# Kernel tuning notes

Measured on AMD Instinct MI355X. Metric: run time of the kernel, lower is better.

## Reference

```python
import jax, jax.numpy as jnp
import numpy as np

DIM = 1024
B, S = 4, 4096

def setup_inputs() -> dict:
    key = jax.random.key(0)
    ks = jax.random.split(key, 8)
    scale = 1.0 / np.sqrt(DIM)
    x = jax.random.normal(ks[0], (B, S, DIM), dtype=jnp.float32)
    Wk = jax.random.normal(ks[1], (DIM, DIM), dtype=jnp.float32) * scale
    Wv = jax.random.normal(ks[2], (DIM, DIM), dtype=jnp.float32) * scale
    Wr = jax.random.normal(ks[3], (DIM, DIM), dtype=jnp.float32) * scale
    Wo = jax.random.normal(ks[4], (DIM, DIM), dtype=jnp.float32) * scale
    time_decay = jax.random.normal(ks[5], (DIM,), dtype=jnp.float32) * 0.01 - 5.0
    time_first = jax.random.normal(ks[6], (DIM,), dtype=jnp.float32) * 0.01
    return {"x": x, "Wk": Wk, "Wv": Wv, "Wr": Wr, "Wo": Wo,
            "time_decay": time_decay, "time_first": time_first}

def reference(x, Wk, Wv, Wr, Wo, time_decay, time_first):
    # Projections (Linear with weight [out, in]: y = x @ W^T)
    k = jnp.einsum('bsd,ed->bse', x, Wk)
    v = jnp.einsum('bsd,ed->bse', x, Wv)
    r = jax.nn.sigmoid(jnp.einsum('bsd,ed->bse', x, Wr))
    w = -jnp.exp(time_decay)          # (D,)
    decay = jnp.exp(w)                # exp(w), per-channel decay in (0,1)
    eu = jnp.exp(time_first)          # exp(u)
    kv = k * v                        # (B, S, D)

    def step(state, kv_t):
        wkv = state + eu * kv_t       # output numerator this step
        new_state = decay * state + kv_t
        return new_state, wkv

    state0 = jnp.zeros((x.shape[0], x.shape[2]), dtype=x.dtype)
    # scan over time axis: move S to leading dim
    _, wkv_seq = jax.lax.scan(step, state0, jnp.swapaxes(kv, 0, 1))  # (S, B, D)
    out = r * jnp.swapaxes(wkv_seq, 0, 1)  # (B, S, D)
    return jnp.einsum('bsd,ed->bse', out, Wo)
```

## Files before the change

### kernel.cpp

```cpp
#include <hip/hip_runtime.h>
#include <hip/hip_bf16.h>

#define DIMD   1024
#define BATCH  4
#define SEQ    4096
#define NTOK   (BATCH * SEQ)
#define CHUNK  64
#define NCHUNK (SEQ / CHUNK)

#define BM 128
#define BN 128
#define BK 32

typedef unsigned short ushort_t;
typedef __attribute__((ext_vector_type(8))) __bf16   bf16x8;
typedef __attribute__((ext_vector_type(4))) float    f32x4;
typedef __attribute__((ext_vector_type(8))) ushort_t u16x8;

__device__ __forceinline__ float b2f(ushort_t u) {
    union { unsigned int i; float f; } x;
    x.i = ((unsigned int)u) << 16;
    return x.f;
}

__device__ __forceinline__ ushort_t f2b(float f) {
    union { float f; unsigned int i; } x;
    x.f = f;
    unsigned int r = x.i + 0x7fffu + ((x.i >> 16) & 1u);
    return (ushort_t)(r >> 16);
}

__global__ __launch_bounds__(256)
void conv_f2b(const float* __restrict__ src, ushort_t* __restrict__ dst, int n8)
{
    const int i = blockIdx.x * 256 + threadIdx.x;
    if (i >= n8) return;
    const float4* s4 = (const float4*)src;
    const float4 a = s4[i * 2];
    const float4 b = s4[i * 2 + 1];
    u16x8 o;
    o[0] = f2b(a.x); o[1] = f2b(a.y); o[2] = f2b(a.z); o[3] = f2b(a.w);
    o[4] = f2b(b.x); o[5] = f2b(b.y); o[6] = f2b(b.z); o[7] = f2b(b.w);
    *(u16x8*)(dst + (size_t)i * 8) = o;
}

__global__ __launch_bounds__(256, 2)
void gemm_kv(const ushort_t* __restrict__ A,
             const ushort_t* __restrict__ Wk,
             const ushort_t* __restrict__ Wv,
             ushort_t* __restrict__ Okv)
{
    __shared__ __align__(16) ushort_t As[BM * BK];
    __shared__ __align__(16) ushort_t Bk[BN * BK];
    __shared__ __align__(16) ushort_t Bv[BN * BK];

    const int tid  = threadIdx.x;
    const int lane = tid & 63;
    const int wv   = tid >> 6;
    const int wr   = wv >> 1;
    const int wc   = wv & 1;
    const int lrow = lane & 15;
    const int kq   = lane >> 4;

    const int row0 = blockIdx.x * BM;
    const int e0   = blockIdx.y * BN;

    f32x4 ak[4][4], av[4][4];
#pragma unroll
    for (int i = 0; i < 4; i++)
#pragma unroll
        for (int j = 0; j < 4; j++) {
            ak[i][j] = f32x4{0.f, 0.f, 0.f, 0.f};
            av[i][j] = f32x4{0.f, 0.f, 0.f, 0.f};
        }

    for (int kt = 0; kt < DIMD / BK; ++kt) {
        const int k0 = kt * BK;

        __syncthreads();

#pragma unroll
        for (int it = 0; it < 2; ++it) {
            const int chunk = tid + it * 256;
            const int r = chunk >> 2;
            const int c = (chunk & 3) << 3;
            const ushort_t* ga = A  + (size_t)(row0 + r) * DIMD + k0 + c;
            const ushort_t* gk = Wk + (size_t)(e0 + r) * DIMD + k0 + c;
            const ushort_t* gv = Wv + (size_t)(e0 + r) * DIMD + k0 + c;
            __builtin_amdgcn_global_load_lds(
                (__attribute__((address_space(1))) void*)ga,
                (__attribute__((address_space(3))) void*)((char*)As + chunk * 16),
                16, 0, 0);
            __builtin_amdgcn_global_load_lds(
                (__attribute__((address_space(1))) void*)gk,
                (__attribute__((address_space(3))) void*)((char*)Bk + chunk * 16),
                16, 0, 0);
            __builtin_amdgcn_global_load_lds(
                (__attribute__((address_space(1))) void*)gv,
                (__attribute__((address_space(3))) void*)((char*)Bv + chunk * 16),
                16, 0, 0);
        }

        __syncthreads();

        bf16x8 af[4], bk4[4], bv4[4];
#pragma unroll
        for (int i = 0; i < 4; i++)
            af[i] = *(const bf16x8*)(As + (wr * 64 + i * 16 + lrow) * BK + kq * 8);
#pragma unroll
        for (int j = 0; j < 4; j++) {
            bk4[j] = *(const bf16x8*)(Bk + (wc * 64 + j * 16 + lrow) * BK + kq * 8);
            bv4[j] = *(const bf16x8*)(Bv + (wc * 64 + j * 16 + lrow) * BK + kq * 8);
        }

#pragma unroll
        for (int i = 0; i < 4; i++)
#pragma unroll
            for (int j = 0; j < 4; j++) {
                ak[i][j] = __builtin_amdgcn_mfma_f32_16x16x32_bf16(
                    af[i], bk4[j], ak[i][j], 0, 0, 0);
                av[i][j] = __builtin_amdgcn_mfma_f32_16x16x32_bf16(
                    af[i], bv4[j], av[i][j], 0, 0, 0);
            }
    }

#pragma unroll
    for (int i = 0; i < 4; i++)
#pragma unroll
        for (int j = 0; j < 4; j++)
#pragma unroll
            for (int r = 0; r < 4; r++) {
                const int row = row0 + wr * 64 + i * 16 + kq * 4 + r;
                const int col = e0 + wc * 64 + j * 16 + lrow;
                Okv[(size_t)row * DIMD + col] = f2b(ak[i][j][r] * av[i][j][r]);
            }
}

template <int SIG, int F32OUT>
__global__ __launch_bounds__(256, 2)
void gemm_bt(const ushort_t* __restrict__ A,
             const ushort_t* __restrict__ W,
             ushort_t* __restrict__ Ob,
             float* __restrict__ Of)
{
    __shared__ __align__(16) ushort_t As[BM * BK];
    __shared__ __align__(16) ushort_t Bs[BN * BK];

    const int tid  = threadIdx.x;
    const int lane = tid & 63;
    const int wv   = tid >> 6;
    const int wr   = wv >> 1;
    const int wc   = wv & 1;
    const int lrow = lane & 15;
    const int kq   = lane >> 4;

    const int row0 = blockIdx.x * BM;
    const int e0   = blockIdx.y * BN;

    f32x4 acc[4][4];
#pragma unroll
    for (int i = 0; i < 4; i++)
#pragma unroll
        for (int j = 0; j < 4; j++)
            acc[i][j] = f32x4{0.f, 0.f, 0.f, 0.f};

    for (int kt = 0; kt < DIMD / BK; ++kt) {
        const int k0 = kt * BK;

        __syncthreads();

#pragma unroll
        for (int it = 0; it < 2; ++it) {
            const int chunk = tid + it * 256;
            const int r = chunk >> 2;
            const int c = (chunk & 3) << 3;
            const ushort_t* ga = A + (size_t)(row0 + r) * DIMD + k0 + c;
            const ushort_t* gb = W + (size_t)(e0 + r) * DIMD + k0 + c;
            __builtin_amdgcn_global_load_lds(
                (__attribute__((address_space(1))) void*)ga,
                (__attribute__((address_space(3))) void*)((char*)As + chunk * 16),
                16, 0, 0);
            __builtin_amdgcn_global_load_lds(
                (__attribute__((address_space(1))) void*)gb,
                (__attribute__((address_space(3))) void*)((char*)Bs + chunk * 16),
                16, 0, 0);
        }

        __syncthreads();

        bf16x8 af[4], bfr[4];
#pragma unroll
        for (int i = 0; i < 4; i++)
            af[i] = *(const bf16x8*)(As + (wr * 64 + i * 16 + lrow) * BK + kq * 8);
#pragma unroll
        for (int j = 0; j < 4; j++)
            bfr[j] = *(const bf16x8*)(Bs + (wc * 64 + j * 16 + lrow) * BK + kq * 8);

#pragma unroll
        for (int i = 0; i < 4; i++)
#pragma unroll
            for (int j = 0; j < 4; j++)
                acc[i][j] = __builtin_amdgcn_mfma_f32_16x16x32_bf16(
                    af[i], bfr[j], acc[i][j], 0, 0, 0);
    }

#pragma unroll
    for (int i = 0; i < 4; i++)
#pragma unroll
        for (int j = 0; j < 4; j++)
#pragma unroll
            for (int r = 0; r < 4; r++) {
                const int row = row0 + wr * 64 + i * 16 + kq * 4 + r;
                const int col = e0 + wc * 64 + j * 16 + lrow;
                float val = acc[i][j][r];
                if (F32OUT) {
                    Of[(size_t)row * DIMD + col] = val;
                } else {
                    if (SIG) val = 1.f / (1.f + __expf(-val));
                    Ob[(size_t)row * DIMD + col] = f2b(val);
                }
            }
}

__global__ __launch_bounds__(256)
void chunk_agg(const ushort_t* __restrict__ kvb,
               const float* __restrict__ td, float* __restrict__ cs)
{
    const int idx = blockIdx.x * 256 + threadIdx.x;
    const int d  = idx & (DIMD - 1);
    const int bc = idx >> 10;
    const int c  = bc & (NCHUNK - 1);
    const int b  = bc >> 6;

    const float decay = __expf(-__expf(td[d]));

    size_t off = ((size_t)b * SEQ + (size_t)c * CHUNK) * DIMD + d;
    float s = 0.f;
#pragma unroll 8
    for (int i = 0; i < CHUNK; i++) {
        s = decay * s + b2f(kvb[off]);
        off += DIMD;
    }
    cs[idx] = s;
}

__global__ __launch_bounds__(256)
void chunk_scan(float* __restrict__ cs, const float* __restrict__ td)
{
    const int idx = blockIdx.x * 256 + threadIdx.x;
    const int d = idx & (DIMD - 1);
    const int b = idx >> 10;

    const float w      = -__expf(td[d]);
    const float decayL = __expf(w * (float)CHUNK);

    float st = 0.f;
    for (int c = 0; c < NCHUNK; c++) {
        const size_t o = ((size_t)b * NCHUNK + c) * DIMD + d;
        const float sc = cs[o];
        cs[o] = st;
        st = decayL * st + sc;
    }
}

__global__ __launch_bounds__(256)
void emit(const ushort_t* __restrict__ kvb, const ushort_t* __restrict__ rb,
          const float* __restrict__ td, const float* __restrict__ tf,
          const float* __restrict__ cs, ushort_t* __restrict__ op)
{
    const int idx = blockIdx.x * 256 + threadIdx.x;
    const int d  = idx & (DIMD - 1);
    const int bc = idx >> 10;
    const int c  = bc & (NCHUNK - 1);
    const int b  = bc >> 6;

    const float decay = __expf(-__expf(td[d]));
    const float eu    = __expf(tf[d]);

    float st = cs[idx];
    size_t off = ((size_t)b * SEQ + (size_t)c * CHUNK) * DIMD + d;
#pragma unroll 8
    for (int i = 0; i < CHUNK; i++) {
        const float kv = b2f(kvb[off]);
        const float rr = b2f(rb[off]);
        op[off] = f2b(rr * (st + eu * kv));
        st = decay * st + kv;
        off += DIMD;
    }
}

extern "C" void kernel_launch(void* const* d_in, const int* in_sizes, int n_in,
                              void* d_out, int out_size, void* d_ws, size_t ws_size,
                              hipStream_t stream)
{
    const float* x  = (const float*)d_in[0];
    const float* Wk = (const float*)d_in[1];
    const float* Wv = (const float*)d_in[2];
    const float* Wr = (const float*)d_in[3];
    const float* Wo = (const float*)d_in[4];
    const float* td = (const float*)d_in[5];
    const float* tf = (const float*)d_in[6];

    ushort_t* xb   = (ushort_t*)d_ws;
    ushort_t* Wkb  = xb  + (size_t)NTOK * DIMD;
    ushort_t* Wvb  = Wkb + (size_t)DIMD * DIMD;
    ushort_t* Wrb  = Wvb + (size_t)DIMD * DIMD;
    ushort_t* Wob  = Wrb + (size_t)DIMD * DIMD;
    float*    cs   = (float*)(Wob + (size_t)DIMD * DIMD);
    ushort_t* pbuf = xb;

    ushort_t* kvb = (ushort_t*)d_out;
    ushort_t* rb  = kvb + (size_t)NTOK * DIMD;
    float*    out = (float*)d_out;

    conv_f2b<<<(NTOK * DIMD / 8 + 255) / 256, 256, 0, stream>>>(x, xb, NTOK * DIMD / 8);
    conv_f2b<<<(DIMD * DIMD / 8 + 255) / 256, 256, 0, stream>>>(Wk, Wkb, DIMD * DIMD / 8);
    conv_f2b<<<(DIMD * DIMD / 8 + 255) / 256, 256, 0, stream>>>(Wv, Wvb, DIMD * DIMD / 8);
    conv_f2b<<<(DIMD * DIMD / 8 + 255) / 256, 256, 0, stream>>>(Wr, Wrb, DIMD * DIMD / 8);
    conv_f2b<<<(DIMD * DIMD / 8 + 255) / 256, 256, 0, stream>>>(Wo, Wob, DIMD * DIMD / 8);

    gemm_kv<<<dim3(NTOK / BM, DIMD / BN), 256, 0, stream>>>(xb, Wkb, Wvb, kvb);

    gemm_bt<1, 0><<<dim3(NTOK / BM, DIMD / BN), 256, 0, stream>>>(xb, Wrb, rb, nullptr);

    chunk_agg<<<(BATCH * NCHUNK * DIMD) / 256, 256, 0, stream>>>(kvb, td, cs);

    chunk_scan<<<(BATCH * DIMD) / 256, 256, 0, stream>>>(cs, td);

    emit<<<(BATCH * NCHUNK * DIMD) / 256, 256, 0, stream>>>(kvb, rb, td, tf, cs, pbuf);

    gemm_bt<0, 1><<<dim3(NTOK / BM, DIMD / BN), 256, 0, stream>>>(pbuf, Wob, nullptr, out);
}
```

Measured before the change: 331.5 us.

## Fuse r projection into kv GEMM, batch weight conversion, vectorize scan kernels

```diff
diff --git a/kernel.cpp b/kernel.cpp
--- a/kernel.cpp
+++ b/kernel.cpp
@@ -44,15 +44,35 @@
     *(u16x8*)(dst + (size_t)i * 8) = o;
 }
 
+__global__ __launch_bounds__(256)
+void conv_w(const float* __restrict__ W0, const float* __restrict__ W1,
+            const float* __restrict__ W2, const float* __restrict__ W3,
+            ushort_t* __restrict__ dst)
+{
+    const int m = blockIdx.y;
+    const float* src = (m == 0) ? W0 : (m == 1) ? W1 : (m == 2) ? W2 : W3;
+    const int i = blockIdx.x * 256 + threadIdx.x;
+    const float4* s4 = (const float4*)src;
+    const float4 a = s4[i * 2];
+    const float4 b = s4[i * 2 + 1];
+    u16x8 o;
+    o[0] = f2b(a.x); o[1] = f2b(a.y); o[2] = f2b(a.z); o[3] = f2b(a.w);
+    o[4] = f2b(b.x); o[5] = f2b(b.y); o[6] = f2b(b.z); o[7] = f2b(b.w);
+    *(u16x8*)(dst + (size_t)m * DIMD * DIMD + (size_t)i * 8) = o;
+}
+
 __global__ __launch_bounds__(256, 2)
-void gemm_kv(const ushort_t* __restrict__ A,
-             const ushort_t* __restrict__ Wk,
-             const ushort_t* __restrict__ Wv,
-             ushort_t* __restrict__ Okv)
+void gemm_kvr(const ushort_t* __restrict__ A,
+              const ushort_t* __restrict__ Wk,
+              const ushort_t* __restrict__ Wv,
+              const ushort_t* __restrict__ Wr,
+              ushort_t* __restrict__ Okv,
+              ushort_t* __restrict__ Or)
 {
     __shared__ __align__(16) ushort_t As[BM * BK];
     __shared__ __align__(16) ushort_t Bk[BN * BK];
     __shared__ __align__(16) ushort_t Bv[BN * BK];
+    __shared__ __align__(16) ushort_t Br[BN * BK];
 
     const int tid  = threadIdx.x;
     const int lane = tid & 63;
@@ -65,13 +85,14 @@
     const int row0 = blockIdx.x * BM;
     const int e0   = blockIdx.y * BN;
 
-    f32x4 ak[4][4], av[4][4];
+    f32x4 ak[4][4], av[4][4], ar[4][4];
 #pragma unroll
     for (int i = 0; i < 4; i++)
 #pragma unroll
         for (int j = 0; j < 4; j++) {
             ak[i][j] = f32x4{0.f, 0.f, 0.f, 0.f};
             av[i][j] = f32x4{0.f, 0.f, 0.f, 0.f};
+            ar[i][j] = f32x4{0.f, 0.f, 0.f, 0.f};
         }
 
     for (int kt = 0; kt < DIMD / BK; ++kt) {
@@ -87,6 +108,7 @@
             const ushort_t* ga = A  + (size_t)(row0 + r) * DIMD + k0 + c;
             const ushort_t* gk = Wk + (size_t)(e0 + r) * DIMD + k0 + c;
             const ushort_t* gv = Wv + (size_t)(e0 + r) * DIMD + k0 + c;
+            const ushort_t* gr = Wr + (size_t)(e0 + r) * DIMD + k0 + c;
             __builtin_amdgcn_global_load_lds(
                 (__attribute__((address_space(1))) void*)ga,
                 (__attribute__((address_space(3))) void*)((char*)As + chunk * 16),
@@ -99,11 +121,15 @@
                 (__attribute__((address_space(1))) void*)gv,
                 (__attribute__((address_space(3))) void*)((char*)Bv + chunk * 16),
                 16, 0, 0);
+            __builtin_amdgcn_global_load_lds(
+                (__attribute__((address_space(1))) void*)gr,
+                (__attribute__((address_space(3))) void*)((char*)Br + chunk * 16),
+                16, 0, 0);
         }
 
         __syncthreads();
 
-        bf16x8 af[4], bk4[4], bv4[4];
+        bf16x8 af[4], bk4[4], bv4[4], br4[4];
 #pragma unroll
         for (int i = 0; i < 4; i++)
             af[i] = *(const bf16x8*)(As + (wr * 64 + i * 16 + lrow) * BK + kq * 8);
@@ -111,6 +137,7 @@
         for (int j = 0; j < 4; j++) {
             bk4[j] = *(const bf16x8*)(Bk + (wc * 64 + j * 16 + lrow) * BK + kq * 8);
             bv4[j] = *(const bf16x8*)(Bv + (wc * 64 + j * 16 + lrow) * BK + kq * 8);
+            br4[j] = *(const bf16x8*)(Br + (wc * 64 + j * 16 + lrow) * BK + kq * 8);
         }
 
 #pragma unroll
@@ -121,6 +148,8 @@
                     af[i], bk4[j], ak[i][j], 0, 0, 0);
                 av[i][j] = __builtin_amdgcn_mfma_f32_16x16x32_bf16(
                     af[i], bv4[j], av[i][j], 0, 0, 0);
+                ar[i][j] = __builtin_amdgcn_mfma_f32_16x16x32_bf16(
+                    af[i], br4[j], ar[i][j], 0, 0, 0);
             }
     }
 
@@ -132,15 +161,15 @@
             for (int r = 0; r < 4; r++) {
                 const int row = row0 + wr * 64 + i * 16 + kq * 4 + r;
                 const int col = e0 + wc * 64 + j * 16 + lrow;
-                Okv[(size_t)row * DIMD + col] = f2b(ak[i][j][r] * av[i][j][r]);
+                const size_t o = (size_t)row * DIMD + col;
+                Okv[o] = f2b(ak[i][j][r] * av[i][j][r]);
+                Or[o]  = f2b(1.f / (1.f + __expf(-ar[i][j][r])));
             }
 }
 
-template <int SIG, int F32OUT>
 __global__ __launch_bounds__(256, 2)
 void gemm_bt(const ushort_t* __restrict__ A,
              const ushort_t* __restrict__ W,
-             ushort_t* __restrict__ Ob,
              float* __restrict__ Of)
 {
     __shared__ __align__(16) ushort_t As[BM * BK];
@@ -212,13 +241,7 @@
             for (int r = 0; r < 4; r++) {
                 const int row = row0 + wr * 64 + i * 16 + kq * 4 + r;
                 const int col = e0 + wc * 64 + j * 16 + lrow;
-                float val = acc[i][j][r];
-                if (F32OUT) {
-                    Of[(size_t)row * DIMD + col] = val;
-                } else {
-                    if (SIG) val = 1.f / (1.f + __expf(-val));
-                    Ob[(size_t)row * DIMD + col] = f2b(val);
-                }
+                Of[(size_t)row * DIMD + col] = acc[i][j][r];
             }
 }
 
@@ -226,22 +249,32 @@
 void chunk_agg(const ushort_t* __restrict__ kvb,
                const float* __restrict__ td, float* __restrict__ cs)
 {
-    const int idx = blockIdx.x * 256 + threadIdx.x;
-    const int d  = idx & (DIMD - 1);
-    const int bc = idx >> 10;
+    const int t  = blockIdx.x * 256 + threadIdx.x;
+    const int d0 = (t & (DIMD / 8 - 1)) * 8;
+    const int bc = t >> 7;
     const int c  = bc & (NCHUNK - 1);
     const int b  = bc >> 6;
 
-    const float decay = __expf(-__expf(td[d]));
-
-    size_t off = ((size_t)b * SEQ + (size_t)c * CHUNK) * DIMD + d;
-    float s = 0.f;
+    float decay[8], s[8];
+#pragma unroll
+    for (int j = 0; j < 8; j++) {
+        decay[j] = __expf(-__expf(td[d0 + j]));
+        s[j] = 0.f;
+    }
+
+    size_t off = ((size_t)b * SEQ + (size_t)c * CHUNK) * DIMD + d0;
 #pragma unroll 8
     for (int i = 0; i < CHUNK; i++) {
-        s = decay * s + b2f(kvb[off]);
+        const u16x8 kv8 = *(const u16x8*)(kvb + off);
+#pragma unroll
+        for (int j = 0; j < 8; j++)
+            s[j] = decay[j] * s[j] + b2f(kv8[j]);
         off += DIMD;
     }
-    cs[idx] = s;
+
+    float* dst = cs + ((size_t)bc * DIMD + d0);
+    *(float4*)(dst)     = float4{s[0], s[1], s[2], s[3]};
+    *(float4*)(dst + 4) = float4{s[4], s[5], s[6], s[7]};
 }
 
 __global__ __launch_bounds__(256)
@@ -254,13 +287,23 @@
     const float w      = -__expf(td[d]);
     const float decayL = __expf(w * (float)CHUNK);
 
+    float v[NCHUNK];
+    const size_t base = ((size_t)b * NCHUNK) * DIMD + d;
+#pragma unroll
+    for (int c = 0; c < NCHUNK; c++)
+        v[c] = cs[base + (size_t)c * DIMD];
+
     float st = 0.f;
+#pragma unroll
     for (int c = 0; c < NCHUNK; c++) {
-        const size_t o = ((size_t)b * NCHUNK + c) * DIMD + d;
-        const float sc = cs[o];
-        cs[o] = st;
+        const float sc = v[c];
+        v[c] = st;
         st = decayL * st + sc;
     }
+
+#pragma unroll
+    for (int c = 0; c < NCHUNK; c++)
+        cs[base + (size_t)c * DIMD] = v[c];
 }
 
 __global__ __launch_bounds__(256)
@@ -268,23 +311,37 @@
           const float* __restrict__ td, const float* __restrict__ tf,
           const float* __restrict__ cs, ushort_t* __restrict__ op)
 {
-    const int idx = blockIdx.x * 256 + threadIdx.x;
-    const int d  = idx & (DIMD - 1);
-    const int bc = idx >> 10;
+    const int t  = blockIdx.x * 256 + threadIdx.x;
+    const int d0 = (t & (DIMD / 8 - 1)) * 8;
+    const int bc = t >> 7;
     const int c  = bc & (NCHUNK - 1);
     const int b  = bc >> 6;
 
-    const float decay = __expf(-__expf(td[d]));
-    const float eu    = __expf(tf[d]);
-
-    float st = cs[idx];
-    size_t off = ((size_t)b * SEQ + (size_t)c * CHUNK) * DIMD + d;
+    float decay[8], eu[8], st[8];
+#pragma unroll
+    for (int j = 0; j < 8; j++) {
+        decay[j] = __expf(-__expf(td[d0 + j]));
+        eu[j]    = __expf(tf[d0 + j]);
+    }
+    const float* csp = cs + ((size_t)bc * DIMD + d0);
+    const float4 s0 = *(const float4*)csp;
+    const float4 s1 = *(const float4*)(csp + 4);
+    st[0] = s0.x; st[1] = s0.y; st[2] = s0.z; st[3] = s0.w;
+    st[4] = s1.x; st[5] = s1.y; st[6] = s1.z; st[7] = s1.w;
+
+    size_t off = ((size_t)b * SEQ + (size_t)c * CHUNK) * DIMD + d0;
 #pragma unroll 8
     for (int i = 0; i < CHUNK; i++) {
-        const float kv = b2f(kvb[off]);
-        const float rr = b2f(rb[off]);
-        op[off] = f2b(rr * (st + eu * kv));
-        st = decay * st + kv;
+        const u16x8 kv8 = *(const u16x8*)(kvb + off);
+        const u16x8 r8  = *(const u16x8*)(rb + off);
+        u16x8 o8;
+#pragma unroll
+        for (int j = 0; j < 8; j++) {
+            const float kv = b2f(kv8[j]);
+            o8[j] = f2b(b2f(r8[j]) * (st[j] + eu[j] * kv));
+            st[j] = decay[j] * st[j] + kv;
+        }
+        *(u16x8*)(op + off) = o8;
         off += DIMD;
     }
 }
@@ -301,33 +358,31 @@
     const float* td = (const float*)d_in[5];
     const float* tf = (const float*)d_in[6];
 
-    ushort_t* xb   = (ushort_t*)d_ws;
-    ushort_t* Wkb  = xb  + (size_t)NTOK * DIMD;
-    ushort_t* Wvb  = Wkb + (size_t)DIMD * DIMD;
-    ushort_t* Wrb  = Wvb + (size_t)DIMD * DIMD;
-    ushort_t* Wob  = Wrb + (size_t)DIMD * DIMD;
-    float*    cs   = (float*)(Wob + (size_t)DIMD * DIMD);
+    ushort_t* xb  = (ushort_t*)d_ws;
+    ushort_t* Wb  = xb + (size_t)NTOK * DIMD;
+    ushort_t* Wkb = Wb;
+    ushort_t* Wvb = Wb + (size_t)DIMD * DIMD;
+    ushort_t* Wrb = Wb + 2 * (size_t)DIMD * DIMD;
+    ushort_t* Wob = Wb + 3 * (size_t)DIMD * DIMD;
+    float*    cs  = (float*)(Wb + 4 * (size_t)DIMD * DIMD);
     ushort_t* pbuf = xb;
 
     ushort_t* kvb = (ushort_t*)d_out;
     ushort_t* rb  = kvb + (size_t)NTOK * DIMD;
     float*    out = (float*)d_out;
 
-    conv_f2b<<<(NTOK * DIMD / 8 + 255) / 256, 256, 0, stream>>>(x, xb, NTOK * DIMD / 8);
-    conv_f2b<<<(DIMD * DIMD / 8 + 255) / 256, 256, 0, stream>>>(Wk, Wkb, DIMD * DIMD / 8);
-    conv_f2b<<<(DIMD * DIMD / 8 + 255) / 256, 256, 0, stream>>>(Wv, Wvb, DIMD * DIMD / 8);
-    conv_f2b<<<(DIMD * DIMD / 8 + 255) / 256, 256, 0, stream>>>(Wr, Wrb, DIMD * DIMD / 8);
-    conv_f2b<<<(DIMD * DIMD / 8 + 255) / 256, 256, 0, stream>>>(Wo, Wob, DIMD * DIMD / 8);
-
-    gemm_kv<<<dim3(NTOK / BM, DIMD / BN), 256, 0, stream>>>(xb, Wkb, Wvb, kvb);
-
-    gemm_bt<1, 0><<<dim3(NTOK / BM, DIMD / BN), 256, 0, stream>>>(xb, Wrb, rb, nullptr);
-
-    chunk_agg<<<(BATCH * NCHUNK * DIMD) / 256, 256, 0, stream>>>(kvb, td, cs);
-
-    chunk_scan<<<(BATCH * DIMD) / 256, 256, 0, stream>>>(cs, td);
-
-    emit<<<(BATCH * NCHUNK * DIMD) / 256, 256, 0, stream>>>(kvb, rb, td, tf, cs, pbuf);
-
-    gemm_bt<0, 1><<<dim3(NTOK / BM, DIMD / BN), 256, 0, stream>>>(pbuf, Wob, nullptr, out);
-}
+    conv_f2b<<<NTOK * DIMD / 8 / 256, 256, 0, stream>>>(x, xb, NTOK * DIMD / 8);
+    conv_w<<<dim3(DIMD * DIMD / 8 / 256, 4), 256, 0, stream>>>(Wk, Wv, Wr, Wo, Wb);
+
+    gemm_kvr<<<dim3(NTOK / BM, DIMD / BN), 256, 0, stream>>>(
+        xb, Wkb, Wvb, Wrb, kvb, rb);
+
+    chunk_agg<<<BATCH * NCHUNK * (DIMD / 8) / 256, 256, 0, stream>>>(kvb, td, cs);
+
+    chunk_scan<<<BATCH * DIMD / 256, 256, 0, stream>>>(cs, td);
+
+    emit<<<BATCH * NCHUNK * (DIMD / 8) / 256, 256, 0, stream>>>(
+        kvb, rb, td, tf, cs, pbuf);
+
+    gemm_bt<<<dim3(NTOK / BM, DIMD / BN), 256, 0, stream>>>(pbuf, Wob, out);
+}
```

Result: slower. 338.9 us (+2.2%).
